# Kernel tuning notes

Hardware: AMD Instinct MI355X
Metric: run time of the kernel (lower is better)

## Reference

```python
import jax, jax.numpy as jnp
import numpy as np

DIM = 192
WINDOW = 7
HEADS = 6
N = WINDOW * WINDOW
B_ = 8192


def _relative_position_index(ws):
    coords = np.stack(np.meshgrid(np.arange(ws), np.arange(ws), indexing='ij'))  # [2, ws, ws]
    coords = coords.reshape(2, -1)                     # [2, ws*ws]
    rel = coords[:, :, None] - coords[:, None, :]      # [2, N, N]
    rel = rel.transpose(1, 2, 0).copy()                # [N, N, 2]
    rel[:, :, 0] += ws - 1
    rel[:, :, 1] += ws - 1
    rel[:, :, 0] *= 2 * ws - 1
    return rel.sum(-1)                                 # [N, N] int


def setup_inputs() -> dict:
    key = jax.random.key(0)
    ks = jax.random.split(key, 6)
    x = jax.random.normal(ks[0], (B_, N, DIM), dtype=jnp.float32)
    # torch Linear weights stored as [in, out] here (y = x @ W + b), same math as x @ W_t.T
    qkv_w = jax.random.normal(ks[1], (DIM, 3 * DIM), dtype=jnp.float32) * (DIM ** -0.5)
    qkv_b = jnp.zeros((3 * DIM,), dtype=jnp.float32)
    proj_w = jax.random.normal(ks[2], (DIM, DIM), dtype=jnp.float32) * (DIM ** -0.5)
    proj_b = jnp.zeros((DIM,), dtype=jnp.float32)
    bias_table = 0.02 * jax.random.normal(ks[3], ((2 * WINDOW - 1) ** 2, HEADS), dtype=jnp.float32)
    rel_idx = jnp.asarray(_relative_position_index(WINDOW), dtype=jnp.int32)  # [N, N]
    return {"x": x, "qkv_w": qkv_w, "qkv_b": qkv_b, "proj_w": proj_w,
            "proj_b": proj_b, "bias_table": bias_table, "rel_idx": rel_idx}


def reference(x, qkv_w, qkv_b, proj_w, proj_b, bias_table, rel_idx):
    B, n, C = x.shape
    H = HEADS
    hd = C // H
    scale = hd ** -0.5
    qkv = x @ qkv_w + qkv_b                         # [B, N, 3C]
    qkv = qkv.reshape(B, n, 3, H, hd)
    q = qkv[:, :, 0].transpose(0, 2, 1, 3)          # [B, H, N, hd]
    k = qkv[:, :, 1].transpose(0, 2, 1, 3)
    v = qkv[:, :, 2].transpose(0, 2, 1, 3)
    attn = jnp.einsum('bhnd,bhmd->bhnm', q, k) * scale  # [B, H, N, N]
    # gathered relative position bias: [N, N, H] -> [H, N, N]
    bias = bias_table[rel_idx].transpose(2, 0, 1)
    attn = attn + bias[None]
    attn = jax.nn.softmax(attn, axis=-1)
    out = jnp.einsum('bhnm,bhmd->bhnd', attn, v)    # [B, H, N, hd]
    out = out.transpose(0, 2, 1, 3).reshape(B, n, C)
    return out @ proj_w + proj_b
```

## Files before the change

### kernel.cpp

```cpp
#include <hip/hip_runtime.h>

#define NW   8192
#define NT   49
#define CDIM 192
#define NH   6
#define HD   32

typedef __attribute__((ext_vector_type(4))) float f32x4;
typedef __attribute__((ext_vector_type(8))) short bf16x8;

__device__ __forceinline__ unsigned short f2b(float f) {
  union { float f; unsigned u; } v; v.f = f;
  unsigned r = v.u + 0x7fffu + ((v.u >> 16) & 1u);
  return (unsigned short)(r >> 16);
}
__device__ __forceinline__ float b2f(unsigned short u) {
  union { unsigned u; float f; } v; v.u = ((unsigned)u) << 16; return v.f;
}

struct __align__(16) Smem {
  unsigned short xb[NT][200];
  unsigned short Ob[NT][200];
  unsigned short qg[64][72];
  unsigned short kg[64][72];
  unsigned short vT[64][72];
  unsigned short P [64][72];
};

__global__ void prep_w(const float* __restrict__ qkv_w, const float* __restrict__ qkv_b,
                       const float* __restrict__ proj_w,
                       unsigned short* __restrict__ wT, unsigned short* __restrict__ projT,
                       float* __restrict__ qb) {
  int idx = blockIdx.x * 256 + threadIdx.x;
  const float scale = 0.17677669529663687f;
  if (idx < 576 * 192) {
    int n = idx / 192, c = idx % 192;
    float v = qkv_w[c * 576 + n];
    if (n < 192) v *= scale;
    wT[idx] = f2b(v);
  } else if (idx < 576 * 192 + 192 * 192) {
    int j = idx - 576 * 192;
    int n = j / 192, c = j % 192;
    projT[j] = f2b(proj_w[c * 192 + n]);
  } else if (idx < 576 * 192 + 192 * 192 + 576) {
    int n = idx - (576 * 192 + 192 * 192);
    float v = qkv_b[n];
    if (n < 192) v *= scale;
    qb[n] = v;
  }
}

__global__ void prep_bias(const float* __restrict__ table, const int* __restrict__ rel,
                          unsigned short* __restrict__ biasF) {
  int idx = blockIdx.x * 256 + threadIdx.x;
  if (idx >= NH * 4 * 4 * 64 * 4) return;
  int reg = idx & 3, lane = (idx >> 2) & 63, jt = (idx >> 8) & 3,
      it = (idx >> 10) & 3, h = idx >> 12;
  int i = it * 16 + (lane >> 4) * 4 + reg;
  int j = jt * 16 + (lane & 15);
  float v = -1e30f;
  if (i < NT && j < NT) v = table[rel[i * NT + j] * NH + h];
  biasF[idx] = f2b(v);
}

__global__ __launch_bounds__(256, 2) void fused_winattn(
    const float* __restrict__ x, const float* __restrict__ projb,
    const unsigned short* __restrict__ wT, const unsigned short* __restrict__ projT,
    const float* __restrict__ qb, const unsigned short* __restrict__ biasF,
    float* __restrict__ out) {
  __shared__ Smem sm;
  const int tid  = threadIdx.x;
  const int lane = tid & 63;
  const int wave = tid >> 6;
  const int l15  = lane & 15;
  const int quad = lane >> 4;
  const int win  = blockIdx.x;

  {
    int4 z = {0, 0, 0, 0};
    int4* p = (int4*)&sm.Ob[0][0];
    for (int i = tid; i < (int)(sizeof(sm.Ob) / 16); i += 256) p[i] = z;
  }
  const float* xw = x + (size_t)win * (NT * CDIM);
  for (int idx = tid; idx < NT * CDIM / 4; idx += 256) {
    int row = idx / 48, c4 = idx % 48;
    float4 v = ((const float4*)xw)[idx];
    ushort4 pk; pk.x = f2b(v.x); pk.y = f2b(v.y); pk.z = f2b(v.z); pk.w = f2b(v.w);
    *(ushort4*)&sm.xb[row][c4 * 4] = pk;
  }
  __syncthreads();

  const int it = wave;

  for (int g = 0; g < 3; ++g) {
    #pragma unroll
    for (int sec = 0; sec < 3; ++sec) {
      const int f0 = sec * CDIM + g * 64 + wave * 16;
      const unsigned short* wrow = wT + (size_t)(f0 + l15) * CDIM + quad * 8;
      bf16x8 wf[6];
      #pragma unroll
      for (int k2 = 0; k2 < 6; ++k2) wf[k2] = *(const bf16x8*)(wrow + k2 * 32);

      if (sec < 2) {
        float4 bq = *(const float4*)(qb + f0 + quad * 4);
        unsigned short* dstb = (sec == 0) ? &sm.qg[0][0] : &sm.kg[0][0];
        #pragma unroll
        for (int tt = 0; tt < 4; ++tt) {
          const unsigned short* xrow = &sm.xb[0][0] + (size_t)(tt * 16 + l15) * 200 + quad * 8;
          f32x4 acc = {0.f, 0.f, 0.f, 0.f};
          #pragma unroll
          for (int k2 = 0; k2 < 6; ++k2)
            acc = __builtin_amdgcn_mfma_f32_16x16x32_bf16(
                wf[k2], *(const bf16x8*)(xrow + k2 * 32), acc, 0, 0, 0);
          acc[0] += bq.x; acc[1] += bq.y; acc[2] += bq.z; acc[3] += bq.w;
          int tok = tt * 16 + l15;
          ushort4 pk;
          if (tok < NT) {
            pk.x = f2b(acc[0]); pk.y = f2b(acc[1]); pk.z = f2b(acc[2]); pk.w = f2b(acc[3]);
          } else { pk.x = pk.y = pk.z = pk.w = 0; }
          *(ushort4*)(dstb + (size_t)tok * 72 + wave * 16 + quad * 4) = pk;
        }
      } else {
        float bv = qb[f0 + l15];
        #pragma unroll
        for (int tt = 0; tt < 4; ++tt) {
          const unsigned short* xrow = &sm.xb[0][0] + (size_t)(tt * 16 + l15) * 200 + quad * 8;
          f32x4 acc = {0.f, 0.f, 0.f, 0.f};
          #pragma unroll
          for (int k2 = 0; k2 < 6; ++k2)
            acc = __builtin_amdgcn_mfma_f32_16x16x32_bf16(
                *(const bf16x8*)(xrow + k2 * 32), wf[k2], acc, 0, 0, 0);
          int j0 = tt * 16 + quad * 4;
          ushort4 pk;
          pk.x = (j0 + 0 < NT) ? f2b(acc[0] + bv) : (unsigned short)0;
          pk.y = (j0 + 1 < NT) ? f2b(acc[1] + bv) : (unsigned short)0;
          pk.z = (j0 + 2 < NT) ? f2b(acc[2] + bv) : (unsigned short)0;
          pk.w = (j0 + 3 < NT) ? f2b(acc[3] + bv) : (unsigned short)0;
          *(ushort4*)(&sm.vT[0][0] + (size_t)(wave * 16 + l15) * 72 + j0) = pk;
        }
      }
    }
    __syncthreads();

    #pragma unroll
    for (int hl = 0; hl < 2; ++hl) {
      const int h = g * 2 + hl;
      bf16x8 aq = *(const bf16x8*)(&sm.qg[0][0] + (size_t)(it * 16 + l15) * 72 + hl * 32 + quad * 8);
      f32x4 s[4];
      #pragma unroll
      for (int jt = 0; jt < 4; ++jt) {
        bf16x8 bk = *(const bf16x8*)(&sm.kg[0][0] + (size_t)(jt * 16 + l15) * 72 + hl * 32 + quad * 8);
        f32x4 z = {0.f, 0.f, 0.f, 0.f};
        s[jt] = __builtin_amdgcn_mfma_f32_16x16x32_bf16(aq, bk, z, 0, 0, 0);
        ushort4 bb = *(const ushort4*)(biasF + ((((h * 4 + it) * 4 + jt) * 64) + lane) * 4);
        s[jt][0] += b2f(bb.x); s[jt][1] += b2f(bb.y);
        s[jt][2] += b2f(bb.z); s[jt][3] += b2f(bb.w);
      }
      float e[4][4], sinv[4];
      #pragma unroll
      for (int r = 0; r < 4; ++r) {
        float e0 = __expf(s[0][r]), e1 = __expf(s[1][r]);
        float e2 = __expf(s[2][r]), e3 = __expf(s[3][r]);
        e[0][r] = e0; e[1][r] = e1; e[2][r] = e2; e[3][r] = e3;
        float sum = (e0 + e1) + (e2 + e3);
        #pragma unroll
        for (int off = 1; off < 16; off <<= 1) sum += __shfl_xor(sum, off, 16);
        sinv[r] = __builtin_amdgcn_rcpf(sum);
      }
      #pragma unroll
      for (int jt = 0; jt < 4; ++jt)
        #pragma unroll
        for (int r = 0; r < 4; ++r)
          sm.P[it * 16 + quad * 4 + r][jt * 16 + l15] = f2b(e[jt][r]);
      bf16x8 ap0 = *(const bf16x8*)(&sm.P[0][0] + (size_t)(it * 16 + l15) * 72 + quad * 8);
      bf16x8 ap1 = *(const bf16x8*)(&sm.P[0][0] + (size_t)(it * 16 + l15) * 72 + 32 + quad * 8);
      #pragma unroll
      for (int dt = 0; dt < 2; ++dt) {
        const unsigned short* vrow = &sm.vT[0][0] + (size_t)(hl * 32 + dt * 16 + l15) * 72;
        bf16x8 bv0 = *(const bf16x8*)(vrow + quad * 8);
        bf16x8 bv1 = *(const bf16x8*)(vrow + 32 + quad * 8);
        f32x4 o = {0.f, 0.f, 0.f, 0.f};
        o = __builtin_amdgcn_mfma_f32_16x16x32_bf16(ap0, bv0, o, 0, 0, 0);
        o = __builtin_amdgcn_mfma_f32_16x16x32_bf16(ap1, bv1, o, 0, 0, 0);
        #pragma unroll
        for (int r = 0; r < 4; ++r) {
          int i = it * 16 + quad * 4 + r;
          if (i < NT)
            sm.Ob[i][h * HD + dt * 16 + l15] = f2b(o[r] * sinv[r]);
        }
      }
    }
    __syncthreads();
  }

  for (int nn = 0; nn < 3; ++nn) {
    int nt = wave + nn * 4;
    int n0 = nt * 16;
    const unsigned short* wrow = projT + (size_t)(n0 + l15) * CDIM + quad * 8;
    bf16x8 bw[6];
    #pragma unroll
    for (int k = 0; k < 6; ++k) bw[k] = *(const bf16x8*)(wrow + k * 32);
    float pb = projb[n0 + l15];
    #pragma unroll
    for (int mt = 0; mt < 4; ++mt) {
      f32x4 acc = {0.f, 0.f, 0.f, 0.f};
      #pragma unroll
      for (int k = 0; k < 6; ++k) {
        bf16x8 ao = *(const bf16x8*)(&sm.Ob[0][0] + (size_t)(mt * 16 + l15) * 200 + k * 32 + quad * 8);
        acc = __builtin_amdgcn_mfma_f32_16x16x32_bf16(ao, bw[k], acc, 0, 0, 0);
      }
      int i0 = mt * 16 + quad * 4;
      #pragma unroll
      for (int r = 0; r < 4; ++r) {
        int i = i0 + r;
        if (i < NT)
          out[((size_t)win * NT + i) * CDIM + n0 + l15] = acc[r] + pb;
      }
    }
  }
}

extern "C" void kernel_launch(void* const* d_in, const int* in_sizes, int n_in,
                              void* d_out, int out_size, void* d_ws, size_t ws_size,
                              hipStream_t stream) {
  const float* x      = (const float*)d_in[0];
  const float* qkv_w  = (const float*)d_in[1];
  const float* qkv_b  = (const float*)d_in[2];
  const float* proj_w = (const float*)d_in[3];
  const float* proj_b = (const float*)d_in[4];
  const float* table  = (const float*)d_in[5];
  const int*   rel    = (const int*)d_in[6];
  float* out = (float*)d_out;

  char* ws = (char*)d_ws;
  unsigned short* wT    = (unsigned short*)(ws);
  unsigned short* projT = (unsigned short*)(ws + 221184);
  float*          qb    = (float*)(ws + 221184 + 73728);
  unsigned short* biasF = (unsigned short*)(ws + 221184 + 73728 + 2304);

  prep_w<<<579, 256, 0, stream>>>(qkv_w, qkv_b, proj_w, wT, projT, qb);
  prep_bias<<<96, 256, 0, stream>>>(table, rel, biasF);
  fused_winattn<<<NW, 256, 0, stream>>>(x, proj_b, wT, projT, qb, biasF, out);
}
```

Measured before the change: 916.8 us.

## Use 8 waves per window and XOR-swizzle attention LDS tiles

Doubles the block to 512 threads. The two wave groups split Q/K projection, the V token halves, the two heads of each group, and the output-projection row tiles, and each group gets its own P buffer. The q/k/v/P tiles move from padded 72-column rows to 64-column rows with an XOR swizzle, which is meant to avoid LDS bank conflicts while using less shared memory. Launch bounds go from (256,2) to (512,4), which tightens the register budget per thread and risks spills.

```diff
diff --git a/kernel.cpp b/kernel.cpp
--- a/kernel.cpp
+++ b/kernel.cpp
@@ -18,13 +18,20 @@
   union { unsigned u; float f; } v; v.u = ((unsigned)u) << 16; return v.f;
 }
 
+__device__ __forceinline__ unsigned short* swz(unsigned short* base, int row, int colU) {
+  return (unsigned short*)((char*)base + row * 128 + (((colU * 2) ^ ((row & 7) << 4))));
+}
+__device__ __forceinline__ const unsigned short* swzc(const unsigned short* base, int row, int colU) {
+  return (const unsigned short*)((const char*)base + row * 128 + (((colU * 2) ^ ((row & 7) << 4))));
+}
+
 struct __align__(16) Smem {
   unsigned short xb[NT][200];
   unsigned short Ob[NT][200];
-  unsigned short qg[64][72];
-  unsigned short kg[64][72];
-  unsigned short vT[64][72];
-  unsigned short P [64][72];
+  unsigned short qg[64][64];
+  unsigned short kg[64][64];
+  unsigned short vT[64][64];
+  unsigned short P2[2][64][64];
 };
 
 __global__ void prep_w(const float* __restrict__ qkv_w, const float* __restrict__ qkv_b,
@@ -63,7 +70,7 @@
   biasF[idx] = f2b(v);
 }
 
-__global__ __launch_bounds__(256, 2) void fused_winattn(
+__global__ __launch_bounds__(512, 4) void fused_winattn(
     const float* __restrict__ x, const float* __restrict__ projb,
     const unsigned short* __restrict__ wT, const unsigned short* __restrict__ projT,
     const float* __restrict__ qb, const unsigned short* __restrict__ biasF,
@@ -79,10 +86,10 @@
   {
     int4 z = {0, 0, 0, 0};
     int4* p = (int4*)&sm.Ob[0][0];
-    for (int i = tid; i < (int)(sizeof(sm.Ob) / 16); i += 256) p[i] = z;
+    for (int i = tid; i < (int)(sizeof(sm.Ob) / 16); i += 512) p[i] = z;
   }
   const float* xw = x + (size_t)win * (NT * CDIM);
-  for (int idx = tid; idx < NT * CDIM / 4; idx += 256) {
+  for (int idx = tid; idx < NT * CDIM / 4; idx += 512) {
     int row = idx / 48, c4 = idx % 48;
     float4 v = ((const float4*)xw)[idx];
     ushort4 pk; pk.x = f2b(v.x); pk.y = f2b(v.y); pk.z = f2b(v.z); pk.w = f2b(v.w);
@@ -90,66 +97,71 @@
   }
   __syncthreads();
 
-  const int it = wave;
+  const int ft  = wave & 3;
+  const int grp = wave >> 2;
+  const int it  = ft;
+  const int hl  = grp;
 
   for (int g = 0; g < 3; ++g) {
-    #pragma unroll
-    for (int sec = 0; sec < 3; ++sec) {
-      const int f0 = sec * CDIM + g * 64 + wave * 16;
-      const unsigned short* wrow = wT + (size_t)(f0 + l15) * CDIM + quad * 8;
-      bf16x8 wf[6];
-      #pragma unroll
-      for (int k2 = 0; k2 < 6; ++k2) wf[k2] = *(const bf16x8*)(wrow + k2 * 32);
-
-      if (sec < 2) {
-        float4 bq = *(const float4*)(qb + f0 + quad * 4);
-        unsigned short* dstb = (sec == 0) ? &sm.qg[0][0] : &sm.kg[0][0];
-        #pragma unroll
-        for (int tt = 0; tt < 4; ++tt) {
-          const unsigned short* xrow = &sm.xb[0][0] + (size_t)(tt * 16 + l15) * 200 + quad * 8;
-          f32x4 acc = {0.f, 0.f, 0.f, 0.f};
-          #pragma unroll
-          for (int k2 = 0; k2 < 6; ++k2)
-            acc = __builtin_amdgcn_mfma_f32_16x16x32_bf16(
-                wf[k2], *(const bf16x8*)(xrow + k2 * 32), acc, 0, 0, 0);
-          acc[0] += bq.x; acc[1] += bq.y; acc[2] += bq.z; acc[3] += bq.w;
-          int tok = tt * 16 + l15;
+    {
+      const int fqk = grp * CDIM + g * 64 + ft * 16;
+      const int fv  = 2 * CDIM + g * 64 + ft * 16;
+      const unsigned short* wr1 = wT + (size_t)(fqk + l15) * CDIM + quad * 8;
+      const unsigned short* wr2 = wT + (size_t)(fv  + l15) * CDIM + quad * 8;
+      bf16x8 wqk[6], wv[6];
+      #pragma unroll
+      for (int k = 0; k < 6; ++k) wqk[k] = *(const bf16x8*)(wr1 + k * 32);
+      #pragma unroll
+      for (int k = 0; k < 6; ++k) wv[k]  = *(const bf16x8*)(wr2 + k * 32);
+      float4 bqk = *(const float4*)(qb + fqk + quad * 4);
+      float  bvs = qb[fv + l15];
+      unsigned short* dqk = grp ? &sm.kg[0][0] : &sm.qg[0][0];
+
+      #pragma unroll
+      for (int tt = 0; tt < 4; ++tt) {
+        const unsigned short* xrow = &sm.xb[0][0] + (size_t)(tt * 16 + l15) * 200 + quad * 8;
+        bf16x8 xf[6];
+        #pragma unroll
+        for (int k = 0; k < 6; ++k) xf[k] = *(const bf16x8*)(xrow + k * 32);
+        const bool dov = ((tt >> 1) == grp);
+        f32x4 a1 = {0.f, 0.f, 0.f, 0.f};
+        f32x4 a2 = {0.f, 0.f, 0.f, 0.f};
+        #pragma unroll
+        for (int k = 0; k < 6; ++k) {
+          a1 = __builtin_amdgcn_mfma_f32_16x16x32_bf16(wqk[k], xf[k], a1, 0, 0, 0);
+          if (dov)
+            a2 = __builtin_amdgcn_mfma_f32_16x16x32_bf16(xf[k], wv[k], a2, 0, 0, 0);
+        }
+        int tok = tt * 16 + l15;
+        {
           ushort4 pk;
           if (tok < NT) {
-            pk.x = f2b(acc[0]); pk.y = f2b(acc[1]); pk.z = f2b(acc[2]); pk.w = f2b(acc[3]);
+            pk.x = f2b(a1[0] + bqk.x); pk.y = f2b(a1[1] + bqk.y);
+            pk.z = f2b(a1[2] + bqk.z); pk.w = f2b(a1[3] + bqk.w);
           } else { pk.x = pk.y = pk.z = pk.w = 0; }
-          *(ushort4*)(dstb + (size_t)tok * 72 + wave * 16 + quad * 4) = pk;
-        }
-      } else {
-        float bv = qb[f0 + l15];
-        #pragma unroll
-        for (int tt = 0; tt < 4; ++tt) {
-          const unsigned short* xrow = &sm.xb[0][0] + (size_t)(tt * 16 + l15) * 200 + quad * 8;
-          f32x4 acc = {0.f, 0.f, 0.f, 0.f};
-          #pragma unroll
-          for (int k2 = 0; k2 < 6; ++k2)
-            acc = __builtin_amdgcn_mfma_f32_16x16x32_bf16(
-                *(const bf16x8*)(xrow + k2 * 32), wf[k2], acc, 0, 0, 0);
+          *(ushort4*)swz(dqk, tok, ft * 16 + quad * 4) = pk;
+        }
+        if (dov) {
           int j0 = tt * 16 + quad * 4;
           ushort4 pk;
-          pk.x = (j0 + 0 < NT) ? f2b(acc[0] + bv) : (unsigned short)0;
-          pk.y = (j0 + 1 < NT) ? f2b(acc[1] + bv) : (unsigned short)0;
-          pk.z = (j0 + 2 < NT) ? f2b(acc[2] + bv) : (unsigned short)0;
-          pk.w = (j0 + 3 < NT) ? f2b(acc[3] + bv) : (unsigned short)0;
-          *(ushort4*)(&sm.vT[0][0] + (size_t)(wave * 16 + l15) * 72 + j0) = pk;
+          pk.x = (j0 + 0 < NT) ? f2b(a2[0] + bvs) : (unsigned short)0;
+          pk.y = (j0 + 1 < NT) ? f2b(a2[1] + bvs) : (unsigned short)0;
+          pk.z = (j0 + 2 < NT) ? f2b(a2[2] + bvs) : (unsigned short)0;
+          pk.w = (j0 + 3 < NT) ? f2b(a2[3] + bvs) : (unsigned short)0;
+          *(ushort4*)swz(&sm.vT[0][0], ft * 16 + l15, j0) = pk;
         }
       }
     }
     __syncthreads();
 
-    #pragma unroll
-    for (int hl = 0; hl < 2; ++hl) {
+    {
       const int h = g * 2 + hl;
-      bf16x8 aq = *(const bf16x8*)(&sm.qg[0][0] + (size_t)(it * 16 + l15) * 72 + hl * 32 + quad * 8);
+      unsigned short* Pb = &sm.P2[hl][0][0];
+      bf16x8 aq = *(const bf16x8*)swzc(&sm.qg[0][0], it * 16 + l15, hl * 32 + quad * 8);
       f32x4 s[4];
       #pragma unroll
       for (int jt = 0; jt < 4; ++jt) {
-        bf16x8 bk = *(const bf16x8*)(&sm.kg[0][0] + (size_t)(jt * 16 + l15) * 72 + hl * 32 + quad * 8);
+        bf16x8 bk = *(const bf16x8*)swzc(&sm.kg[0][0], jt * 16 + l15, hl * 32 + quad * 8);
         f32x4 z = {0.f, 0.f, 0.f, 0.f};
         s[jt] = __builtin_amdgcn_mfma_f32_16x16x32_bf16(aq, bk, z, 0, 0, 0);
         ushort4 bb = *(const ushort4*)(biasF + ((((h * 4 + it) * 4 + jt) * 64) + lane) * 4);
@@ -171,14 +183,13 @@
       for (int jt = 0; jt < 4; ++jt)
         #pragma unroll
         for (int r = 0; r < 4; ++r)
-          sm.P[it * 16 + quad * 4 + r][jt * 16 + l15] = f2b(e[jt][r]);
-      bf16x8 ap0 = *(const bf16x8*)(&sm.P[0][0] + (size_t)(it * 16 + l15) * 72 + quad * 8);
-      bf16x8 ap1 = *(const bf16x8*)(&sm.P[0][0] + (size_t)(it * 16 + l15) * 72 + 32 + quad * 8);
+          *swz(Pb, it * 16 + quad * 4 + r, jt * 16 + l15) = f2b(e[jt][r]);
+      bf16x8 ap0 = *(const bf16x8*)swzc(Pb, it * 16 + l15, quad * 8);
+      bf16x8 ap1 = *(const bf16x8*)swzc(Pb, it * 16 + l15, 32 + quad * 8);
       #pragma unroll
       for (int dt = 0; dt < 2; ++dt) {
-        const unsigned short* vrow = &sm.vT[0][0] + (size_t)(hl * 32 + dt * 16 + l15) * 72;
-        bf16x8 bv0 = *(const bf16x8*)(vrow + quad * 8);
-        bf16x8 bv1 = *(const bf16x8*)(vrow + 32 + quad * 8);
+        bf16x8 bv0 = *(const bf16x8*)swzc(&sm.vT[0][0], hl * 32 + dt * 16 + l15, quad * 8);
+        bf16x8 bv1 = *(const bf16x8*)swzc(&sm.vT[0][0], hl * 32 + dt * 16 + l15, 32 + quad * 8);
         f32x4 o = {0.f, 0.f, 0.f, 0.f};
         o = __builtin_amdgcn_mfma_f32_16x16x32_bf16(ap0, bv0, o, 0, 0, 0);
         o = __builtin_amdgcn_mfma_f32_16x16x32_bf16(ap1, bv1, o, 0, 0, 0);
@@ -193,28 +204,31 @@
     __syncthreads();
   }
 
-  for (int nn = 0; nn < 3; ++nn) {
-    int nt = wave + nn * 4;
-    int n0 = nt * 16;
-    const unsigned short* wrow = projT + (size_t)(n0 + l15) * CDIM + quad * 8;
-    bf16x8 bw[6];
+  {
     #pragma unroll
-    for (int k = 0; k < 6; ++k) bw[k] = *(const bf16x8*)(wrow + k * 32);
-    float pb = projb[n0 + l15];
-    #pragma unroll
-    for (int mt = 0; mt < 4; ++mt) {
-      f32x4 acc = {0.f, 0.f, 0.f, 0.f};
-      #pragma unroll
-      for (int k = 0; k < 6; ++k) {
-        bf16x8 ao = *(const bf16x8*)(&sm.Ob[0][0] + (size_t)(mt * 16 + l15) * 200 + k * 32 + quad * 8);
-        acc = __builtin_amdgcn_mfma_f32_16x16x32_bf16(ao, bw[k], acc, 0, 0, 0);
-      }
-      int i0 = mt * 16 + quad * 4;
-      #pragma unroll
-      for (int r = 0; r < 4; ++r) {
-        int i = i0 + r;
-        if (i < NT)
-          out[((size_t)win * NT + i) * CDIM + n0 + l15] = acc[r] + pb;
+    for (int mm = 0; mm < 2; ++mm) {
+      int mt = grp * 2 + mm;
+      bf16x8 ao[6];
+      #pragma unroll
+      for (int k = 0; k < 6; ++k)
+        ao[k] = *(const bf16x8*)(&sm.Ob[0][0] + (size_t)(mt * 16 + l15) * 200 + k * 32 + quad * 8);
+      #pragma unroll
+      for (int nn = 0; nn < 3; ++nn) {
+        int n0 = (ft + nn * 4) * 16;
+        const unsigned short* wrow = projT + (size_t)(n0 + l15) * CDIM + quad * 8;
+        f32x4 acc = {0.f, 0.f, 0.f, 0.f};
+        #pragma unroll
+        for (int k = 0; k < 6; ++k)
+          acc = __builtin_amdgcn_mfma_f32_16x16x32_bf16(
+              ao[k], *(const bf16x8*)(wrow + k * 32), acc, 0, 0, 0);
+        float pb = projb[n0 + l15];
+        int i0 = mt * 16 + quad * 4;
+        #pragma unroll
+        for (int r = 0; r < 4; ++r) {
+          int i = i0 + r;
+          if (i < NT)
+            out[((size_t)win * NT + i) * CDIM + n0 + l15] = acc[r] + pb;
+        }
       }
     }
   }
@@ -240,5 +254,5 @@
 
   prep_w<<<579, 256, 0, stream>>>(qkv_w, qkv_b, proj_w, wT, projT, qb);
   prep_bias<<<96, 256, 0, stream>>>(table, rel, biasF);
-  fused_winattn<<<NW, 256, 0, stream>>>(x, proj_b, wT, projT, qb, biasF, out);
-}
+  fused_winattn<<<NW, 512, 0, stream>>>(x, proj_b, wT, projT, qb, biasF, out);
+}
```

Result: slower. 1.042 ms (+13.6%).
